# Optimization experiments

Measured on AMD Instinct MI355X. Metric: run time of the kernel, lower is better.

## Reference

```python
import jax, jax.numpy as jnp
import numpy as np

B, S, D, H, E = 4, 2048, 512, 8, 4  # batch, seq, embed, heads, expand
HD = D // H


def setup_inputs() -> dict:
    key = jax.random.key(0)
    ks = jax.random.split(key, 9)
    s = lambda k, shape, fan: jax.random.normal(k, shape, jnp.float32) * (fan ** -0.5)
    return {
        "x": jax.random.normal(ks[0], (B, S, D), jnp.float32),
        "Wq": s(ks[1], (D, D), D),
        "Wk": s(ks[2], (D, D), D),
        "Wv": s(ks[3], (D, D), D),
        "Wo": s(ks[4], (D, D), D),
        "W1": s(ks[5], (D, D * E), D),
        "b1": jnp.zeros((D * E,), jnp.float32),
        "W2": s(ks[6], (D * E, D), D * E),
        "b2": jnp.zeros((D,), jnp.float32),
    }


def _encoder_layer(x, Wq, Wk, Wv, Wo, W1, b1, W2, b2):
    # NOTE: source computes InstanceNorm1d twice but discards both results -> no-ops.
    scale = D ** -0.25  # applied to BOTH q and k (net 1/sqrt(embed_dim))
    q = (x @ Wq).reshape(B, S, H, HD).transpose(0, 2, 1, 3) * scale  # [B,H,S,hd]
    k = (x @ Wk).reshape(B, S, H, HD).transpose(0, 2, 1, 3) * scale
    v = (x @ Wv).reshape(B, S, H, HD).transpose(0, 2, 1, 3)
    scores = jnp.einsum('bhqd,bhkd->bhqk', q, k)  # [B,H,S,S]
    attn = jax.nn.softmax(scores, axis=-1)
    o = jnp.einsum('bhqk,bhkd->bhqd', attn, v)  # [B,H,S,hd]
    o = o.transpose(0, 2, 1, 3).reshape(B, S, D)
    x = o @ Wo + x  # residual 1
    h = jax.nn.gelu(x @ W1 + b1, approximate=True)  # torch GELU(approximate='tanh')
    return h @ W2 + b2 + x  # residual 2 (dropout=0, eval)


def reference(x, Wq, Wk, Wv, Wo, W1, b1, W2, b2):
    return _encoder_layer(x, Wq, Wk, Wv, Wo, W1, b1, W2, b2)
```

## Files before the change

kernel.cpp:

```cpp
#include <hip/hip_runtime.h>
#include <hip/hip_bf16.h>


typedef __bf16 bf16;
typedef __attribute__((ext_vector_type(8))) __bf16 bf16x8;
typedef __attribute__((ext_vector_type(4))) __bf16 bf16x4;
typedef __attribute__((ext_vector_type(4))) float f32x4;
typedef __attribute__((ext_vector_type(16))) float f32x16;
typedef __attribute__((ext_vector_type(4))) short s16x4;

#define LOG2E 1.4426950408889634f
#define SCORE_SCALE 0.044194173824159216f
#define SCALE_L2E (SCORE_SCALE * LOG2E)
#define FIXED_M 12.0f

#if __has_builtin(__builtin_amdgcn_exp2f)
#define EXP2(x) __builtin_amdgcn_exp2f(x)
#else
#define EXP2(x) exp2f(x)
#endif

__device__ __forceinline__ void gl_lds16(const bf16* g, bf16* l) {
  __builtin_amdgcn_global_load_lds(
      (const __attribute__((address_space(1))) unsigned int*)g,
      (__attribute__((address_space(3))) unsigned int*)l, 16, 0, 0);
}

__device__ __forceinline__ float gelu_tanh(float x) {
  float u = 0.7978845608028654f * (x + 0.044715f * x * x * x);
  float e = EXP2(u * (2.0f * LOG2E));
  float th = 1.0f - 2.0f / (e + 1.0f);
  return 0.5f * x * (1.0f + th);
}

__device__ __forceinline__ f32x4 mfma_bf16(bf16x8 a, bf16x8 b, f32x4 c) {
  return __builtin_amdgcn_mfma_f32_16x16x32_bf16(a, b, c, 0, 0, 0);
}
__device__ __forceinline__ f32x16 mfma32x16(bf16x8 a, bf16x8 b, f32x16 c) {
  return __builtin_amdgcn_mfma_f32_32x32x16_bf16(a, b, c, 0, 0, 0);
}
__device__ __forceinline__ f32x16 mfma32x8(bf16x4 a, bf16x4 b, f32x16 c) {
#if __has_builtin(__builtin_amdgcn_mfma_f32_32x32x8_bf16)
  return __builtin_amdgcn_mfma_f32_32x32x8_bf16(a, b, c, 0, 0, 0);
#else
  return __builtin_amdgcn_mfma_f32_32x32x8bf16_1k(
      __builtin_bit_cast(s16x4, a), __builtin_bit_cast(s16x4, b), c, 0, 0, 0);
#endif
}

template <int MODE, typename OutT, int TN>
__global__ __launch_bounds__(256, 2) void gemm_bt(
    const bf16* __restrict__ A, const bf16* __restrict__ Bt,
    OutT* __restrict__ C, const float* __restrict__ bias,
    const float* __restrict__ resf, const bf16* __restrict__ resb,
    int M, int N, int K) {
  constexpr int MI = (TN == 128) ? 4 : 2;
  __shared__ __align__(16) bf16 sA[2][128 * 32];
  __shared__ __align__(16) bf16 sB[2][TN * 32];
  const int tid = threadIdx.x;
  const int lane = tid & 63;
  const int quad = lane >> 4, lc = lane & 15;
  const int wave = tid >> 6;
  const int wr = (TN == 128) ? (wave >> 1) : wave;
  const int wc = (TN == 128) ? (wave & 1) : 0;
  const int m0 = blockIdx.y * 128, n0 = blockIdx.x * TN;

  const int srow = tid >> 2;
  const int kc = (tid & 3) * 8;
  const bf16* Ag1 = A + (size_t)(m0 + srow) * K + kc;
  const bf16* Ag2 = A + (size_t)(m0 + 64 + srow) * K + kc;
  const bf16* Bg1 = Bt + (size_t)(n0 + srow) * K + kc;
  const bf16* Bg2 = Bt + (size_t)(n0 + 64 + srow) * K + kc;
  const int o1 = tid * 8, o2 = (tid + 256) * 8;

  f32x4 acc[MI][4];
#pragma unroll
  for (int mi = 0; mi < MI; ++mi)
#pragma unroll
    for (int ni = 0; ni < 4; ++ni) acc[mi][ni] = (f32x4){0.f, 0.f, 0.f, 0.f};

  gl_lds16(Ag1, sA[0] + o1);
  gl_lds16(Ag2, sA[0] + o2);
  gl_lds16(Bg1, sB[0] + o1);
  if (TN == 128) gl_lds16(Bg2, sB[0] + o2);
  Ag1 += 32; Ag2 += 32; Bg1 += 32; Bg2 += 32;

  const int kIters = K >> 5;
  for (int kt = 0; kt < kIters; ++kt) {
    __syncthreads();
    const bf16* cA = sA[kt & 1];
    const bf16* cB = sB[kt & 1];
    if (kt + 1 < kIters) {
      bf16* nA = sA[(kt + 1) & 1];
      bf16* nB = sB[(kt + 1) & 1];
      gl_lds16(Ag1, nA + o1);
      gl_lds16(Ag2, nA + o2);
      gl_lds16(Bg1, nB + o1);
      if (TN == 128) gl_lds16(Bg2, nB + o2);
      Ag1 += 32; Ag2 += 32; Bg1 += 32; Bg2 += 32;
    }

    bf16x8 af[MI], bfm[4];
#pragma unroll
    for (int i = 0; i < MI; ++i)
      af[i] =
          *(const bf16x8*)(cA + ((wr * (16 * MI) + i * 16 + lc) * 32 + quad * 8));
#pragma unroll
    for (int i = 0; i < 4; ++i)
      bfm[i] = *(const bf16x8*)(cB + ((wc * 64 + i * 16 + lc) * 32 + quad * 8));
#pragma unroll
    for (int mi = 0; mi < MI; ++mi)
#pragma unroll
      for (int ni = 0; ni < 4; ++ni)
        acc[mi][ni] = mfma_bf16(af[mi], bfm[ni], acc[mi][ni]);
  }

#pragma unroll
  for (int mi = 0; mi < MI; ++mi) {
#pragma unroll
    for (int r = 0; r < 4; ++r) {
      const int row = m0 + wr * (16 * MI) + mi * 16 + quad * 4 + r;
#pragma unroll
      for (int ni = 0; ni < 4; ++ni) {
        const int col = n0 + wc * 64 + ni * 16 + lc;
        const size_t idx = (size_t)row * N + col;
        float v = acc[mi][ni][r];
        if (MODE == 1) v += resf[idx];
        if (MODE == 2) v = gelu_tanh(v + bias[col]);
        if (MODE == 3) v += bias[col] + (float)resb[idx];
        C[idx] = (OutT)v;
      }
    }
  }
}

__global__ __launch_bounds__(256, 2) void flash_attn(
    const bf16* __restrict__ QKV, const bf16* __restrict__ Vt,
    bf16* __restrict__ O) {
  const int tid = threadIdx.x;
  const int lane = tid & 63, wave = tid >> 6;
  const int lo5 = lane & 31, hi = lane >> 5;
  const int bh = blockIdx.y, b = bh >> 3, h = bh & 7;
  const int q0 = blockIdx.x * 128 + wave * 32;

  __shared__ __align__(16) bf16 sK[2][4096];
  __shared__ __align__(16) bf16 sV[2][4096];

  const bf16* Qrow = QKV + (size_t)(b * 2048 + q0 + lo5) * 1536 + h * 64;
  bf16x8 qf[4];
#pragma unroll
  for (int i = 0; i < 4; ++i) qf[i] = *(const bf16x8*)(Qrow + i * 16 + hi * 8);

  const int colsw = (((lane & 7) ^ (lane >> 3)) << 3);
  const bf16* Kg = QKV + (size_t)b * 2048 * 1536 + 512 + (size_t)h * 64 +
                   (size_t)(wave * 16 + (lane >> 3)) * 1536 + colsw;
  const bf16* Vg = Vt + (size_t)bh * 64 * 2048 +
                   (size_t)(wave * 16 + (lane >> 3)) * 2048 + colsw;
  const int stag = wave * 1024;

  const int m7 = lo5 & 7;

  f32x16 oacc[2];
  oacc[0] = (f32x16)(0.f);
  oacc[1] = (f32x16)(0.f);
  float rsum = 0.f;

  gl_lds16(Kg, sK[0] + stag);
  gl_lds16(Kg + 8 * 1536, sK[0] + stag + 512);
  gl_lds16(Vg, sV[0] + stag);
  gl_lds16(Vg + 8 * 2048, sV[0] + stag + 512);
  Kg += (size_t)64 * 1536;

  for (int kt = 0; kt < 32; ++kt) {
    __syncthreads();
    const bf16* cK = sK[kt & 1];
    const bf16* cV = sV[kt & 1];
    if (kt < 31) {
      bf16* nK = sK[(kt + 1) & 1];
      bf16* nV = sV[(kt + 1) & 1];
      gl_lds16(Kg, nK + stag);
      gl_lds16(Kg + 8 * 1536, nK + stag + 512);
      gl_lds16(Vg + (kt + 1) * 64, nV + stag);
      gl_lds16(Vg + (kt + 1) * 64 + 8 * 2048, nV + stag + 512);
      Kg += (size_t)64 * 1536;
    }

    bf16x4 pa[2][4];
#pragma unroll
    for (int hl = 0; hl < 2; ++hl) {
      f32x16 st = (f32x16)(0.f);
#pragma unroll
      for (int i = 0; i < 4; ++i) {
        const int R = hl * 32 + lo5;
        bf16x8 kf =
            *(const bf16x8*)(cK + R * 64 + (((2 * i + hi) ^ m7) << 3));
        st = mfma32x16(kf, qf[i], st);
      }
#pragma unroll
      for (int g = 0; g < 4; ++g) {
        bf16x4 pb;
#pragma unroll
        for (int j = 0; j < 4; ++j) {
          float p = EXP2(st[4 * g + j] * SCALE_L2E - FIXED_M);
          rsum += p;
          pb[j] = (bf16)p;
        }
        pa[hl][g] = pb;
      }
    }

#pragma unroll
    for (int dh = 0; dh < 2; ++dh) {
      const int Rd = dh * 32 + lo5;
#pragma unroll
      for (int ks = 0; ks < 8; ++ks) {
        bf16x4 vf =
            *(const bf16x4*)(cV + Rd * 64 + (((ks ^ m7)) << 3) + hi * 4);
        oacc[dh] = mfma32x8(pa[ks >> 2][ks & 3], vf, oacc[dh]);
      }
    }
  }

  rsum += __shfl_xor(rsum, 32, 64);
  const size_t obase = (size_t)(b * 2048 + q0) * 512 + h * 64;
#pragma unroll
  for (int r = 0; r < 16; ++r) {
    const int qloc = (r & 3) + 8 * (r >> 2) + 4 * hi;
    const float inv = 1.0f / __shfl(rsum, qloc, 64);
#pragma unroll
    for (int dh = 0; dh < 2; ++dh)
      O[obase + (size_t)qloc * 512 + dh * 32 + lo5] =
          (bf16)(oacc[dh][r] * inv);
  }
}

__global__ __launch_bounds__(256) void prep(
    const float* __restrict__ x, const float* __restrict__ Wq,
    const float* __restrict__ Wk, const float* __restrict__ Wv,
    const float* __restrict__ Wo, const float* __restrict__ W1,
    const float* __restrict__ W2, bf16* __restrict__ xb,
    bf16* __restrict__ WqkvT, bf16* __restrict__ WoT, bf16* __restrict__ W1T,
    bf16* __restrict__ W2T) {
  const int bid = blockIdx.x;
  if (bid < 4096) {
    const size_t i = ((size_t)bid * 256 + threadIdx.x) * 4;
    const float4 v = *(const float4*)(x + i);
    bf16x4 o;
    o[0] = (bf16)v.x; o[1] = (bf16)v.y; o[2] = (bf16)v.z; o[3] = (bf16)v.w;
    *(bf16x4*)(xb + i) = o;
    return;
  }
  const int t = bid - 4096;
  const float* in;
  bf16* out;
  int in_ld, out_ld, bx, by;
  if (t < 1024) {
    const int q = t >> 8, r = t & 255;
    bx = r & 15; by = r >> 4; in_ld = 512; out_ld = 512;
    in = (q == 0) ? Wq : (q == 1) ? Wk : (q == 2) ? Wv : Wo;
    out = (q == 0) ? WqkvT
          : (q == 1) ? WqkvT + 512 * 512
          : (q == 2) ? WqkvT + 2 * 512 * 512
                     : WoT;
  } else if (t < 2048) {
    const int r = t - 1024;
    bx = r & 63; by = r >> 6; in_ld = 2048; out_ld = 512;
    in = W1; out = W1T;
  } else {
    const int r = t - 2048;
    bx = r & 15; by = r >> 4; in_ld = 512; out_ld = 2048;
    in = W2; out = W2T;
  }
  __shared__ __align__(16) bf16 tl[32][33];
  const int tx = threadIdx.x & 31, ty = threadIdx.x >> 5;
  const int n0 = bx * 32, k0 = by * 32;
#pragma unroll
  for (int i = 0; i < 4; ++i)
    tl[ty + 8 * i][tx] = (bf16)in[(size_t)(k0 + ty + 8 * i) * in_ld + n0 + tx];
  __syncthreads();
#pragma unroll
  for (int i = 0; i < 4; ++i)
    out[(size_t)(n0 + ty + 8 * i) * out_ld + k0 + tx] = tl[tx][ty + 8 * i];
}

__global__ __launch_bounds__(256) void transpose_v(
    const bf16* __restrict__ QKV, bf16* __restrict__ Vt) {
  __shared__ __align__(16) bf16 t[32][33];
  const int tx = threadIdx.x & 31, ty = threadIdx.x >> 5;
  const int bh = blockIdx.z, b = bh >> 3, h = bh & 7;
  const bf16* ip = QKV + (size_t)b * 2048 * 1536 + 1024 + h * 64;
  bf16* op = Vt + (size_t)bh * 64 * 2048;
  const int d0 = blockIdx.x * 32, s0 = blockIdx.y * 32;
#pragma unroll
  for (int i = 0; i < 4; ++i)
    t[ty + 8 * i][tx] = ip[(size_t)(s0 + ty + 8 * i) * 1536 + d0 + tx];
  __syncthreads();
#pragma unroll
  for (int i = 0; i < 4; ++i)
    op[(size_t)(d0 + ty + 8 * i) * 2048 + s0 + tx] = t[tx][ty + 8 * i];
}

extern "C" void kernel_launch(void* const* d_in, const int* in_sizes, int n_in,
                              void* d_out, int out_size, void* d_ws,
                              size_t ws_size, hipStream_t stream) {
  const float* x = (const float*)d_in[0];
  const float* Wq = (const float*)d_in[1];
  const float* Wk = (const float*)d_in[2];
  const float* Wv = (const float*)d_in[3];
  const float* Wo = (const float*)d_in[4];
  const float* W1 = (const float*)d_in[5];
  const float* b1 = (const float*)d_in[6];
  const float* W2 = (const float*)d_in[7];
  const float* b2 = (const float*)d_in[8];
  float* out = (float*)d_out;

  char* ws = (char*)d_ws;
  size_t off = 0;
  auto alloc = [&](size_t bytes) {
    char* p = ws + off;
    off += (bytes + 255) & ~(size_t)255;
    return p;
  };
  bf16* WqkvT = (bf16*)alloc(1536ULL * 512 * 2);
  bf16* WoT = (bf16*)alloc(512ULL * 512 * 2);
  bf16* W1T = (bf16*)alloc(2048ULL * 512 * 2);
  bf16* W2T = (bf16*)alloc(512ULL * 2048 * 2);
  bf16* xb = (bf16*)alloc(8192ULL * 512 * 2);
  bf16* QKV = (bf16*)alloc(8192ULL * 1536 * 2);
  bf16* Vt = (bf16*)alloc(32ULL * 64 * 2048 * 2);
  bf16* attn = (bf16*)alloc(8192ULL * 512 * 2);
  bf16* x2 = xb;
  bf16* hbuf = QKV;

  const dim3 tb(256);
  prep<<<dim3(7168), tb, 0, stream>>>(x, Wq, Wk, Wv, Wo, W1, W2, xb, WqkvT,
                                      WoT, W1T, W2T);
  gemm_bt<0, bf16, 128><<<dim3(12, 64), tb, 0, stream>>>(
      xb, WqkvT, QKV, nullptr, nullptr, nullptr, 8192, 1536, 512);
  transpose_v<<<dim3(2, 64, 32), tb, 0, stream>>>(QKV, Vt);
  flash_attn<<<dim3(16, 32), tb, 0, stream>>>(QKV, Vt, attn);
  gemm_bt<1, bf16, 64><<<dim3(8, 64), tb, 0, stream>>>(
      attn, WoT, x2, nullptr, x, nullptr, 8192, 512, 512);
  gemm_bt<2, bf16, 128><<<dim3(16, 64), tb, 0, stream>>>(
      x2, W1T, hbuf, b1, nullptr, nullptr, 8192, 2048, 512);
  gemm_bt<3, float, 64><<<dim3(8, 64), tb, 0, stream>>>(
      hbuf, W2T, out, b2, nullptr, x2, 8192, 512, 2048);
}
```

Baseline: 264.1 us.

## Triple-buffer flash attention K/V and use 32x32x16 MFMA for PV

Moves K/V staging from a double buffer to a triple buffer, prefetching two tiles ahead, and replaces __syncthreads with an explicit partial vmcnt wait plus s_barrier. The P·V product now uses v_permlane32_swap to rearrange probability fragments so it can run on the wider 32x32x16 bf16 MFMA instead of 32x32x8, halving the MFMA and LDS-read count. It also raises wave priority around MFMA blocks. The costs are more shared memory, which may reduce occupancy, and correctness that depends on the hand-written waitcnt counts and the permlane layout.

```diff
diff --git a/kernel.cpp b/kernel.cpp
--- a/kernel.cpp
+++ b/kernel.cpp
@@ -8,6 +8,8 @@
 typedef __attribute__((ext_vector_type(4))) float f32x4;
 typedef __attribute__((ext_vector_type(16))) float f32x16;
 typedef __attribute__((ext_vector_type(4))) short s16x4;
+typedef __attribute__((ext_vector_type(2))) unsigned int u32x2;
+typedef __attribute__((ext_vector_type(4))) unsigned int u32x4;
 
 #define LOG2E 1.4426950408889634f
 #define SCORE_SCALE 0.044194173824159216f
@@ -39,13 +41,9 @@
 __device__ __forceinline__ f32x16 mfma32x16(bf16x8 a, bf16x8 b, f32x16 c) {
   return __builtin_amdgcn_mfma_f32_32x32x16_bf16(a, b, c, 0, 0, 0);
 }
-__device__ __forceinline__ f32x16 mfma32x8(bf16x4 a, bf16x4 b, f32x16 c) {
-#if __has_builtin(__builtin_amdgcn_mfma_f32_32x32x8_bf16)
-  return __builtin_amdgcn_mfma_f32_32x32x8_bf16(a, b, c, 0, 0, 0);
-#else
-  return __builtin_amdgcn_mfma_f32_32x32x8bf16_1k(
-      __builtin_bit_cast(s16x4, a), __builtin_bit_cast(s16x4, b), c, 0, 0, 0);
-#endif
+
+__device__ __forceinline__ void plswap(unsigned int& a, unsigned int& b) {
+  asm volatile("v_permlane32_swap_b32 %0, %1" : "+v"(a), "+v"(b));
 }
 
 template <int MODE, typename OutT, int TN>
@@ -143,8 +141,8 @@
   const int bh = blockIdx.y, b = bh >> 3, h = bh & 7;
   const int q0 = blockIdx.x * 128 + wave * 32;
 
-  __shared__ __align__(16) bf16 sK[2][4096];
-  __shared__ __align__(16) bf16 sV[2][4096];
+  __shared__ __align__(16) bf16 sK[3][4096];
+  __shared__ __align__(16) bf16 sV[3][4096];
 
   const bf16* Qrow = QKV + (size_t)(b * 2048 + q0 + lo5) * 1536 + h * 64;
   bf16x8 qf[4];
@@ -152,12 +150,11 @@
   for (int i = 0; i < 4; ++i) qf[i] = *(const bf16x8*)(Qrow + i * 16 + hi * 8);
 
   const int colsw = (((lane & 7) ^ (lane >> 3)) << 3);
-  const bf16* Kg = QKV + (size_t)b * 2048 * 1536 + 512 + (size_t)h * 64 +
-                   (size_t)(wave * 16 + (lane >> 3)) * 1536 + colsw;
-  const bf16* Vg = Vt + (size_t)bh * 64 * 2048 +
-                   (size_t)(wave * 16 + (lane >> 3)) * 2048 + colsw;
+  const bf16* Kg0 = QKV + (size_t)b * 2048 * 1536 + 512 + (size_t)h * 64 +
+                    (size_t)(wave * 16 + (lane >> 3)) * 1536 + colsw;
+  const bf16* Vg0 = Vt + (size_t)bh * 64 * 2048 +
+                    (size_t)(wave * 16 + (lane >> 3)) * 2048 + colsw;
   const int stag = wave * 1024;
-
   const int m7 = lo5 & 7;
 
   f32x16 oacc[2];
@@ -165,37 +162,39 @@
   oacc[1] = (f32x16)(0.f);
   float rsum = 0.f;
 
-  gl_lds16(Kg, sK[0] + stag);
-  gl_lds16(Kg + 8 * 1536, sK[0] + stag + 512);
-  gl_lds16(Vg, sV[0] + stag);
-  gl_lds16(Vg + 8 * 2048, sV[0] + stag + 512);
-  Kg += (size_t)64 * 1536;
+  auto stage = [&](int buf, int t) {
+    gl_lds16(Kg0 + (size_t)t * 64 * 1536, sK[buf] + stag);
+    gl_lds16(Kg0 + (size_t)(t * 64 + 8) * 1536, sK[buf] + stag + 512);
+    gl_lds16(Vg0 + t * 64, sV[buf] + stag);
+    gl_lds16(Vg0 + t * 64 + 8 * 2048, sV[buf] + stag + 512);
+  };
+  stage(0, 0);
+  stage(1, 1);
 
   for (int kt = 0; kt < 32; ++kt) {
-    __syncthreads();
-    const bf16* cK = sK[kt & 1];
-    const bf16* cV = sV[kt & 1];
-    if (kt < 31) {
-      bf16* nK = sK[(kt + 1) & 1];
-      bf16* nV = sV[(kt + 1) & 1];
-      gl_lds16(Kg, nK + stag);
-      gl_lds16(Kg + 8 * 1536, nK + stag + 512);
-      gl_lds16(Vg + (kt + 1) * 64, nV + stag);
-      gl_lds16(Vg + (kt + 1) * 64 + 8 * 2048, nV + stag + 512);
-      Kg += (size_t)64 * 1536;
-    }
-
-    bf16x4 pa[2][4];
+    if (kt == 31)
+      asm volatile("s_waitcnt vmcnt(0)\ns_barrier" ::: "memory");
+    else
+      asm volatile("s_waitcnt vmcnt(4)\ns_barrier" ::: "memory");
+    const int cb = kt % 3;
+    const bf16* cK = sK[cb];
+    const bf16* cV = sV[cb];
+    if (kt + 2 < 32) stage((kt + 2) % 3, kt + 2);
+
+    bf16x8 paw[4];
 #pragma unroll
     for (int hl = 0; hl < 2; ++hl) {
       f32x16 st = (f32x16)(0.f);
+      const int R = hl * 32 + lo5;
+      __builtin_amdgcn_s_setprio(1);
 #pragma unroll
       for (int i = 0; i < 4; ++i) {
-        const int R = hl * 32 + lo5;
         bf16x8 kf =
             *(const bf16x8*)(cK + R * 64 + (((2 * i + hi) ^ m7) << 3));
         st = mfma32x16(kf, qf[i], st);
       }
+      __builtin_amdgcn_s_setprio(0);
+      unsigned int q32[4][2];
 #pragma unroll
       for (int g = 0; g < 4; ++g) {
         bf16x4 pb;
@@ -205,20 +204,33 @@
           rsum += p;
           pb[j] = (bf16)p;
         }
-        pa[hl][g] = pb;
+        u32x2 w2 = __builtin_bit_cast(u32x2, pb);
+        q32[g][0] = w2[0];
+        q32[g][1] = w2[1];
+      }
+#pragma unroll
+      for (int t = 0; t < 2; ++t) {
+        unsigned int a0 = q32[2 * t][0], a1 = q32[2 * t][1];
+        unsigned int b0 = q32[2 * t + 1][0], b1 = q32[2 * t + 1][1];
+        plswap(a0, b0);
+        plswap(a1, b1);
+        u32x4 f = {a0, a1, b0, b1};
+        paw[hl * 2 + t] = __builtin_bit_cast(bf16x8, f);
       }
     }
 
+    __builtin_amdgcn_s_setprio(1);
 #pragma unroll
     for (int dh = 0; dh < 2; ++dh) {
       const int Rd = dh * 32 + lo5;
 #pragma unroll
-      for (int ks = 0; ks < 8; ++ks) {
-        bf16x4 vf =
-            *(const bf16x4*)(cV + Rd * 64 + (((ks ^ m7)) << 3) + hi * 4);
-        oacc[dh] = mfma32x8(pa[ks >> 2][ks & 3], vf, oacc[dh]);
+      for (int w = 0; w < 4; ++w) {
+        bf16x8 vf =
+            *(const bf16x8*)(cV + Rd * 64 + (((2 * w + hi) ^ m7) << 3));
+        oacc[dh] = mfma32x16(paw[w], vf, oacc[dh]);
       }
     }
+    __builtin_amdgcn_s_setprio(0);
   }
 
   rsum += __shfl_xor(rsum, 32, 64);
```

Result: faster. 256.6 us (-2.8%).
